# Kernel optimization log

Hardware: AMD Instinct MI355X
Metric: run time of the kernel (lower is better)

Reference implementation:

```python
import jax, jax.numpy as jnp
import numpy as np

# ---- fixed constants from stft2hcfp.__init__ ----
FS = 16000.0; FR = 2.0; FC = 27.5; TC = 1.0 / 4487.0; NPO = 48
N = int(FS / FR)                      # 8000 FFT length
HALF_N = int(round(N / 2))            # 4000
SQRT_N = float(np.sqrt(N))
HIGH_FREQ_IDX = int(round(1.0 / TC / FR) + 1)   # 2245
HIGH_QUEF_IDX = int(round(FS / FC)) + 1         # 583
CUT_Q = int(round(FS * TC))           # 4  (cepstrum cutoff)
TOTAL_BINS = 4 * 88                   # 352 log-freq bins
NUM_HARMONIC = 5

def _central_freqs():
    stop = 1.0 / TC
    nest = int(np.ceil(np.log2(stop / FC)) * NPO)
    cf = []
    for i in range(nest):
        c = FC * 2.0 ** (float(i) / NPO)
        if c < stop:
            cf.append(c)
        else:
            break
    return cf

CF = _central_freqs()   # 353 central frequencies
NEST = len(CF)

def _freq_matrix():
    # triangular log-frequency filterbank over linear freq axis
    f = (FS * np.linspace(0, 0.5, HALF_N, endpoint=True))[:HIGH_FREQ_IDX]
    W = np.zeros((NEST - 1, len(f)), np.float32)
    for i in range(1, NEST - 1):
        l = int(round(CF[i - 1] / FR)); r = int(round(CF[i + 1] / FR) + 1)
        if l >= r - 1:
            W[i, l] = 1.0
        else:
            for j in range(l, r):
                if CF[i - 1] < f[j] < CF[i]:
                    W[i, j] = (f[j] - CF[i - 1]) / (CF[i] - CF[i - 1])
                elif CF[i] < f[j] < CF[i + 1]:
                    W[i, j] = (CF[i + 1] - f[j]) / (CF[i + 1] - CF[i])
    return W

def _quef_matrix():
    q = np.arange(HIGH_QUEF_IDX) / FS + 1e-6
    fq = 1.0 / q
    W = np.zeros((NEST - 1, len(fq)), np.float32)
    for i in range(1, NEST - 1):
        for j in range(int(round(FS / CF[i + 1])), int(round(FS / CF[i - 1]) + 1)):
            if j >= len(fq):
                continue
            if CF[i - 1] < fq[j] < CF[i]:
                W[i, j] = (fq[j] - CF[i - 1]) / (CF[i] - CF[i - 1])
            elif CF[i] < fq[j] < CF[i + 1]:
                W[i, j] = (CF[i + 1] - fq[j]) / (CF[i + 1] - CF[i])
    return W

# harmonic shift indices: closest central freq to (k+1)*27.5 Hz, k=0..5
HIDS = [int(np.argmin(np.abs(np.asarray(CF) - (k + 1) * FC))) for k in range(NUM_HARMONIC + 1)]


def _nonlinear(x, g, cutoff):
    # relu + pow(g), then zero first/last `cutoff` rows along axis 1.
    # safe pow: grad is 0 where x<=0 (matches relu-masked torch behavior, no inf at 0)
    y = jnp.where(x > 0, jnp.where(x > 0, x, 1.0) ** g, 0.0)
    y = y.at[:, :cutoff].set(0.0).at[:, -cutoff:].set(0.0)
    return y


def setup_inputs() -> dict:
    key = jax.random.key(0)
    dx = jax.random.uniform(key, (8, 512, N), dtype=jnp.float32)  # [B, T, 8000] spectrogram
    return {
        "dx": dx,
        "W_freq": jnp.asarray(_freq_matrix()),   # [352, 2245]
        "W_quef": jnp.asarray(_quef_matrix()),   # [352, 583]
    }


def reference(dx, W_freq, W_quef):
    tfr0 = jnp.swapaxes(dx, 1, 2)                       # [B, F=8000, T]
    # CFP layer 1: real part of FFT over freq axis -> cepstrum, nonlinear g=0.6
    ceps = jnp.fft.fft(tfr0, axis=1).real / SQRT_N      # [B, 8000, T]
    ceps = _nonlinear(ceps, 0.6, CUT_Q)
    # log-frequency mappings (banded triangular filterbanks)
    tfr0h = tfr0[:, :HIGH_FREQ_IDX]                      # [B, 2245, T]
    cepsh = ceps[:, :HIGH_QUEF_IDX]                      # [B, 583, T]
    tfrL0 = jnp.einsum('kf,bft->bkt', W_freq, tfr0h)     # [B, 352, T]
    tfrLQ = jnp.einsum('kq,bqt->bkt', W_quef, cepsh)     # [B, 352, T]
    # harmonic stacking: shift down (spectral) / shift up (cepstral)
    har_s = [jnp.pad(tfrL0[:, h:TOTAL_BINS], ((0, 0), (0, h), (0, 0))) for h in HIDS]
    har_c = [jnp.pad(tfrLQ[:, :TOTAL_BINS - h], ((0, 0), (h, 0), (0, 0))) for h in HIDS]
    piece = jnp.concatenate([jnp.stack(har_s, axis=1), jnp.stack(har_c, axis=1)], axis=1)
    return jnp.swapaxes(piece, 2, 3)                     # [B, 12, T, 352]
```

## Files before the change

kernel.cpp:

```cpp
#include <hip/hip_runtime.h>
#include <hip/hip_bf16.h>
#include <limits.h>

typedef __attribute__((ext_vector_type(8))) short short8;
typedef __attribute__((ext_vector_type(4))) float f32x4;
typedef __attribute__((ext_vector_type(16))) float f32x16;

#define NN 8000
#define NCOL 4096
#define KBINS 352
#define QPAD 640
#define QH 320
#define BN 256
#define KC 8
#define NTILE 64
#define KSTEP 8
#define CUTQ 4
#define T_ 512
#define WFB 64
#define WQB 20
#define NGC 2560

#define GLL16(g, l) __builtin_amdgcn_global_load_lds( \
    (const __attribute__((address_space(1))) unsigned int*)(g), \
    (__attribute__((address_space(3))) unsigned int*)(l), 16, 0, 0)

static __device__ __forceinline__ ushort bfc(float f){
  __hip_bfloat16 h = __float2bfloat16(f);
  return *reinterpret_cast<ushort*>(&h);
}
static __device__ __forceinline__ float b2f(ushort u){
  unsigned v = ((unsigned)u) << 16; float f; __builtin_memcpy(&f, &v, 4); return f;
}

#define PADI(j) ((j) + ((j) >> 5))

__global__ __launch_bounds__(512) void prep_k(const float* __restrict__ dx,
        ushort* __restrict__ xf, ushort* __restrict__ cosg,
        const float* __restrict__ Wf, const float* __restrict__ Wq,
        int HFI, int HQI, int* __restrict__ fLo, int* __restrict__ qLo,
        float* __restrict__ WfT, float* __restrict__ WqT){
  __shared__ float sbuf[4232];
  __shared__ int slo, shi;
  int bid = blockIdx.x;
  int t = threadIdx.x;

  if (bid < NCOL){
    int row = bid;
    const float* rp = dx + (size_t)row*NN;
    {
      int j0 = t*8;
      f32x4 v0 = *(const f32x4*)(rp + 3896 + j0);
      f32x4 v1 = *(const f32x4*)(rp + 3896 + j0 + 4);
      #pragma unroll
      for (int e=0;e<4;e++) sbuf[PADI(j0+e)] = v0[e];
      #pragma unroll
      for (int e=0;e<4;e++) sbuf[PADI(j0+4+e)] = v1[e];
      if (t == 0){
        #pragma unroll
        for (int e=0;e<8;e++) sbuf[PADI(4096+e)] = rp[7992+e];
      }
    }
    __syncthreads();
    int n0 = t*8;
    f32x4 p0 = *(const f32x4*)(rp + n0);
    f32x4 p1 = *(const f32x4*)(rp + n0 + 4);
    float pr[8] = {p0[0],p0[1],p0[2],p0[3],p1[0],p1[1],p1[2],p1[3]};
    short8 o;
    #pragma unroll
    for (int e=0;e<8;e++){
      int n = n0 + e;
      float v;
      if (n == 0)          v = pr[0];
      else if (n < 4000)   v = pr[e] + sbuf[PADI(4104 - n)];
      else if (n == 4000)  v = pr[e];
      else                 v = 0.f;
      o[e] = (short)bfc(v);
    }
    int kt = n0 >> 6, s8 = (n0 >> 3) & 7;
    *(short8*)(&xf[((size_t)kt*NCOL + row)*64 + ((s8 ^ (row & 7)) << 3)]) = o;
  } else if (bid < NCOL + NGC){
    int base = (bid - NCOL) * 1024;
    #pragma unroll
    for (int u2=0;u2<2;u2++){
      int id = base + u2*512 + t;
      int q = id >> 12, n = id & 4095;
      float v = 0.f;
      if (q < HQI){
        int m = (q*n) % NN;
        v = cosf((float)m * 7.8539816339744831e-4f);
      }
      int kt = n >> 6, s8 = (n >> 3) & 7, e = n & 7;
      cosg[(size_t)kt*(QPAD*64) + (size_t)q*64 + (((s8 ^ (q & 7)) << 3) | e)] = bfc(v);
    }
  } else {
    int u = bid - NCOL - NGC;
    int r = u >> 1;
    bool isF = (u & 1) == 0;
    const float* W = isF ? Wf : Wq;
    int width = isF ? HFI : HQI;
    int bw    = isF ? WFB : WQB;
    float* WT = isF ? WfT : WqT;
    int* Lo   = isF ? fLo : qLo;
    if (t==0){ slo = INT_MAX; shi = -1; }
    __syncthreads();
    int mylo = INT_MAX, myhi = -1;
    for (int c = t; c < width; c += 512){
      if (W[(size_t)r*width + c] != 0.f){ if (c < mylo) mylo = c; if (c > myhi) myhi = c; }
    }
    atomicMin(&slo, mylo); atomicMax(&shi, myhi);
    __syncthreads();
    int l = (shi < 0) ? 0 : slo, h = (shi < 0) ? 0 : shi + 1;
    if (t==0) Lo[r] = l;
    for (int j = t; j < bw; j += 512){
      float v = 0.f;
      if (l + j < h) v = W[(size_t)r*width + l + j];
      WT[(size_t)j*KBINS + r] = v;
    }
  }
}

__global__ __launch_bounds__(512, 2) void gemm_k(const ushort* __restrict__ xf,
                                                 const ushort* __restrict__ cosg,
                                                 ushort* __restrict__ part){
  __shared__ ushort As[2][QH*64];
  __shared__ ushort Bs[2][BN*64];
  int tid = threadIdx.x;
  int nb = blockIdx.x, qh = blockIdx.y, kc = blockIdx.z;
  int lane = tid & 63, widx = tid >> 6;
  int wm = widx & 1, wn = widx >> 1;
  int l31 = lane & 31, lh = lane >> 5;
  int kt0 = kc*KSTEP, ktE = kt0 + KSTEP;

  const ushort* ag0 = cosg + (size_t)qh*(QH*64) + tid*8;
  const ushort* bg0 = xf + (size_t)nb*(BN*64) + tid*8;

  #define STAGE(kt_, buf_) { \
    const ushort* ag_ = ag0 + (size_t)(kt_)*(QPAD*64); \
    _Pragma("unroll") \
    for (int i_=0;i_<5;i_++) GLL16(ag_ + i_*4096, &As[buf_][tid*8 + i_*4096]); \
    const ushort* bg_ = bg0 + (size_t)(kt_)*(NCOL*64); \
    _Pragma("unroll") \
    for (int i_=0;i_<4;i_++) GLL16(bg_ + i_*4096, &Bs[buf_][tid*8 + i_*4096]); }

  f32x16 acc[5][2];
  #pragma unroll
  for (int a=0;a<5;a++){ acc[a][0] = (f32x16)0.f; acc[a][1] = (f32x16)0.f; }

  STAGE(kt0, 0);

  int cur = 0;
  for (int kt = kt0; kt < ktE; ++kt){
    if (kt + 1 < ktE){
      STAGE(kt+1, cur^1);
      asm volatile("s_waitcnt vmcnt(9)" ::: "memory");
    } else {
      asm volatile("s_waitcnt vmcnt(0)" ::: "memory");
    }
    __builtin_amdgcn_s_barrier();
    __builtin_amdgcn_sched_barrier(0);
    const ushort* Ac = &As[cur][0];
    const ushort* Bc = &Bs[cur][0];
    #pragma unroll
    for (int p=0;p<4;p++){
      short8 dfr[2];
      #pragma unroll
      for (int c=0;c<2;c++){
        int row = wn*64 + c*32 + l31;
        dfr[c] = *(const short8*)(Bc + row*64 + ((((p<<1)|lh) ^ (row & 7)) << 3));
      }
      short8 cfr[5];
      #pragma unroll
      for (int a=0;a<5;a++){
        int row = wm*160 + a*32 + l31;
        cfr[a] = *(const short8*)(Ac + row*64 + ((((p<<1)|lh) ^ (row & 7)) << 3));
      }
      __builtin_amdgcn_s_setprio(1);
      #pragma unroll
      for (int a=0;a<5;a++){
        acc[a][0] = __builtin_amdgcn_mfma_f32_32x32x16_bf16(dfr[0], cfr[a], acc[a][0], 0,0,0);
        acc[a][1] = __builtin_amdgcn_mfma_f32_32x32x16_bf16(dfr[1], cfr[a], acc[a][1], 0,0,0);
      }
      __builtin_amdgcn_s_setprio(0);
      __builtin_amdgcn_sched_barrier(0);
      __builtin_amdgcn_s_barrier();
      __builtin_amdgcn_sched_barrier(0);
    }
    cur ^= 1;
  }

  ushort* pb = part + (size_t)kc*NCOL*QPAD;
  #pragma unroll
  for (int a=0;a<5;a++){
    int q = qh*QH + wm*160 + a*32 + l31;
    #pragma unroll
    for (int c=0;c<2;c++){
      int colb = nb*BN + wn*64 + c*32 + 4*lh;
      #pragma unroll
      for (int r=0;r<16;r++){
        int col = colb + (r&3) + 8*(r>>2);
        pb[(size_t)col*QPAD + q] = bfc(acc[a][c][r]);
      }
    }
  }
}

__global__ __launch_bounds__(384) void fuse_k(const float* __restrict__ dx,
        const ushort* __restrict__ part,
        const float* __restrict__ WfT, const float* __restrict__ WqT,
        const int* __restrict__ fLo, const int* __restrict__ qLo,
        float* __restrict__ out, int HFI, int HQI){
  __shared__ float xr[2368];
  __shared__ float yq[QPAD];
  __shared__ float tl0[KBINS];
  __shared__ float tlq[KBINS];
  int col = blockIdx.x;
  int b = col >> 9, t = col & 511;
  int tid = threadIdx.x;
  const float invs = 0.011180339887498949f;

  for (int f = tid; f < 2368; f += 384) xr[f] = (f < HFI) ? dx[(size_t)col*NN + f] : 0.f;
  const ushort* pc = part + (size_t)col*QPAD;
  for (int q = tid; q < QPAD; q += 384){
    float y = 0.f;
    if (q < HQI){
      float s = 0.f;
      #pragma unroll
      for (int kc=0; kc<KC; kc++) s += b2f(pc[(size_t)kc*NCOL*QPAD + q]);
      s *= invs;
      if (q >= CUTQ && s > 0.f) y = powf(s, 0.6f);
    }
    yq[q] = y;
  }
  __syncthreads();

  if (tid < KBINS){
    int k = tid;
    int lo = fLo[k];
    float aF = 0.f;
    #pragma unroll
    for (int j=0;j<WFB;j++) aF += WfT[j*KBINS + k] * xr[lo + j];
    int ql = qLo[k];
    float aQ = 0.f;
    #pragma unroll
    for (int j=0;j<WQB;j++) aQ += WqT[j*KBINS + k] * yq[ql + j];
    tl0[k] = aF; tlq[k] = aQ;
  }
  __syncthreads();

  const int hids[6] = {0,48,76,96,111,124};
  for (int u = tid; u < 12*KBINS; u += 384){
    int j = u / KBINS;
    int k = u - j*KBINS;
    int h = hids[(j < 6) ? j : j - 6];
    float v;
    if (j < 6) v = (k + h < KBINS) ? tl0[k + h] : 0.f;
    else       v = (k >= h)        ? tlq[k - h] : 0.f;
    out[(((size_t)b*12 + j)*T_ + t)*KBINS + k] = v;
  }
}

extern "C" void kernel_launch(void* const* d_in, const int* in_sizes, int n_in,
                              void* d_out, int out_size, void* d_ws, size_t ws_size,
                              hipStream_t stream){
  const float* dx = (const float*)d_in[0];
  const float* Wf = (const float*)d_in[1];
  const float* Wq = (const float*)d_in[2];
  int HFI = in_sizes[1] / KBINS;
  int HQI = in_sizes[2] / KBINS;
  float* out = (float*)d_out;
  char* ws = (char*)d_ws;

  ushort* cosg = (ushort*)ws;
  size_t off = (size_t)NTILE*QPAD*64*2;
  ushort* xf = (ushort*)(ws + off); off += (size_t)NTILE*NCOL*64*2;
  ushort* part = (ushort*)(ws + off); off += (size_t)KC*NCOL*QPAD*2;
  int* fLo = (int*)(ws+off); off += KBINS*4;
  int* qLo = (int*)(ws+off); off += KBINS*4;
  float* WfT = (float*)(ws+off); off += (size_t)WFB*KBINS*4;
  float* WqT = (float*)(ws+off); off += (size_t)WQB*KBINS*4;
  (void)n_in; (void)out_size; (void)ws_size;

  prep_k<<<NCOL + NGC + 2*KBINS, 512, 0, stream>>>(dx, xf, cosg, Wf, Wq,
                                                   HFI, HQI, fLo, qLo, WfT, WqT);
  gemm_k<<<dim3(NCOL/BN, QPAD/QH, KC), 512, 0, stream>>>(xf, cosg, part);
  fuse_k<<<NCOL, 384, 0, stream>>>(dx, part, WfT, WqT, fLo, qLo, out, HFI, HQI);
}
```

Before: 128.5 us.

## Split prep kernel into cosine, fold, and band-prep kernels with LDS-staged fold

Breaks the monolithic prep kernel into three launches: cosine table generation, an input fold kernel, and filterbank band extraction. The fold kernel now reads the mirrored half directly from global memory with vector loads, with no per-row shared buffer. It handles 8 rows per block and stages the output in LDS, so each write to the tiled xf layout is a contiguous 1KB segment instead of scattered 16-byte stores. The aim is better write coalescing and less branch divergence between block types. The cost is two extra kernel launches.

```diff
diff --git a/kernel.cpp b/kernel.cpp
--- a/kernel.cpp
+++ b/kernel.cpp
@@ -19,7 +19,7 @@
 #define T_ 512
 #define WFB 64
 #define WQB 20
-#define NGC 2560
+#define LTS 528
 
 #define GLL16(g, l) __builtin_amdgcn_global_load_lds( \
     (const __attribute__((address_space(1))) unsigned int*)(g), \
@@ -33,90 +33,87 @@
   unsigned v = ((unsigned)u) << 16; float f; __builtin_memcpy(&f, &v, 4); return f;
 }
 
-#define PADI(j) ((j) + ((j) >> 5))
-
-__global__ __launch_bounds__(512) void prep_k(const float* __restrict__ dx,
-        ushort* __restrict__ xf, ushort* __restrict__ cosg,
-        const float* __restrict__ Wf, const float* __restrict__ Wq,
-        int HFI, int HQI, int* __restrict__ fLo, int* __restrict__ qLo,
-        float* __restrict__ WfT, float* __restrict__ WqT){
-  __shared__ float sbuf[4232];
-  __shared__ int slo, shi;
-  int bid = blockIdx.x;
+__global__ void gen_cos_k(ushort* __restrict__ cosg, int HQI){
+  int n = blockIdx.x*256 + threadIdx.x;
+  int q = blockIdx.y;
+  float v = 0.f;
+  if (q < HQI){
+    int m = (q*n) % NN;
+    v = cosf((float)m * 7.8539816339744831e-4f);
+  }
+  int kt = n >> 6, s8 = (n >> 3) & 7, e = n & 7;
+  cosg[(size_t)kt*(QPAD*64) + (size_t)q*64 + (((s8 ^ (q & 7)) << 3) | e)] = bfc(v);
+}
+
+__global__ __launch_bounds__(512, 2) void fold_k(const float* __restrict__ dx,
+                                                 ushort* __restrict__ xf){
+  __shared__ ushort lbuf[NTILE*LTS];
+  int rg = blockIdx.x;
   int t = threadIdx.x;
-
-  if (bid < NCOL){
-    int row = bid;
-    const float* rp = dx + (size_t)row*NN;
-    {
-      int j0 = t*8;
-      f32x4 v0 = *(const f32x4*)(rp + 3896 + j0);
-      f32x4 v1 = *(const f32x4*)(rp + 3896 + j0 + 4);
-      #pragma unroll
-      for (int e=0;e<4;e++) sbuf[PADI(j0+e)] = v0[e];
-      #pragma unroll
-      for (int e=0;e<4;e++) sbuf[PADI(j0+4+e)] = v1[e];
-      if (t == 0){
-        #pragma unroll
-        for (int e=0;e<8;e++) sbuf[PADI(4096+e)] = rp[7992+e];
-      }
-    }
-    __syncthreads();
-    int n0 = t*8;
+  int w = t >> 6, l = t & 63;
+  int row = rg*8 + w;
+  const float* rp = dx + (size_t)row*NN;
+  int swz = (row & 7) << 3;
+
+  #pragma unroll
+  for (int sub=0; sub<8; ++sub){
+    int n0 = sub*512 + l*8;
     f32x4 p0 = *(const f32x4*)(rp + n0);
     f32x4 p1 = *(const f32x4*)(rp + n0 + 4);
+    f32x4 ma = *(const f32x4*)(rp + 7996 - n0);
+    f32x4 mb = *(const f32x4*)(rp + 7992 - n0);
+    float ms = rp[n0 ? NN - n0 : 0];
     float pr[8] = {p0[0],p0[1],p0[2],p0[3],p1[0],p1[1],p1[2],p1[3]};
+    float mi[8] = {n0 ? ms : 0.f, ma[3],ma[2],ma[1],ma[0],mb[3],mb[2],mb[1]};
     short8 o;
     #pragma unroll
     for (int e=0;e<8;e++){
       int n = n0 + e;
       float v;
       if (n == 0)          v = pr[0];
-      else if (n < 4000)   v = pr[e] + sbuf[PADI(4104 - n)];
+      else if (n < 4000)   v = pr[e] + mi[e];
       else if (n == 4000)  v = pr[e];
       else                 v = 0.f;
       o[e] = (short)bfc(v);
     }
-    int kt = n0 >> 6, s8 = (n0 >> 3) & 7;
-    *(short8*)(&xf[((size_t)kt*NCOL + row)*64 + ((s8 ^ (row & 7)) << 3)]) = o;
-  } else if (bid < NCOL + NGC){
-    int base = (bid - NCOL) * 1024;
-    #pragma unroll
-    for (int u2=0;u2<2;u2++){
-      int id = base + u2*512 + t;
-      int q = id >> 12, n = id & 4095;
-      float v = 0.f;
-      if (q < HQI){
-        int m = (q*n) % NN;
-        v = cosf((float)m * 7.8539816339744831e-4f);
-      }
-      int kt = n >> 6, s8 = (n >> 3) & 7, e = n & 7;
-      cosg[(size_t)kt*(QPAD*64) + (size_t)q*64 + (((s8 ^ (q & 7)) << 3) | e)] = bfc(v);
-    }
-  } else {
-    int u = bid - NCOL - NGC;
-    int r = u >> 1;
-    bool isF = (u & 1) == 0;
-    const float* W = isF ? Wf : Wq;
-    int width = isF ? HFI : HQI;
-    int bw    = isF ? WFB : WQB;
-    float* WT = isF ? WfT : WqT;
-    int* Lo   = isF ? fLo : qLo;
-    if (t==0){ slo = INT_MAX; shi = -1; }
-    __syncthreads();
-    int mylo = INT_MAX, myhi = -1;
-    for (int c = t; c < width; c += 512){
-      if (W[(size_t)r*width + c] != 0.f){ if (c < mylo) mylo = c; if (c > myhi) myhi = c; }
-    }
-    atomicMin(&slo, mylo); atomicMax(&shi, myhi);
-    __syncthreads();
-    int l = (shi < 0) ? 0 : slo, h = (shi < 0) ? 0 : shi + 1;
-    if (t==0) Lo[r] = l;
-    for (int j = t; j < bw; j += 512){
-      float v = 0.f;
-      if (l + j < h) v = W[(size_t)r*width + l + j];
-      WT[(size_t)j*KBINS + r] = v;
-    }
+    int kt = n0 >> 6, s8 = n0 & 56;
+    *(short8*)(&lbuf[kt*LTS + w*64 + (s8 ^ swz)]) = o;
+  }
+  __syncthreads();
+
+  #pragma unroll
+  for (int j=0;j<8;++j){
+    int kt = j*8 + w;
+    short8 v = *(const short8*)(&lbuf[kt*LTS + l*8]);
+    *(short8*)(&xf[((size_t)kt*NCOL + rg*8)*64 + l*8]) = v;
+  }
+}
+
+__global__ void bp_k(const float* __restrict__ Wf, const float* __restrict__ Wq,
+                     int HFI, int HQI, int* __restrict__ fLo, int* __restrict__ qLo,
+                     float* __restrict__ WfT, float* __restrict__ WqT){
+  __shared__ int slo, shi;
+  int r = blockIdx.x;
+  bool isF = (blockIdx.y == 0);
+  const float* W = isF ? Wf : Wq;
+  int width = isF ? HFI : HQI;
+  int bw    = isF ? WFB : WQB;
+  float* WT = isF ? WfT : WqT;
+  int* Lo   = isF ? fLo : qLo;
+  if (threadIdx.x==0){ slo = INT_MAX; shi = -1; }
+  __syncthreads();
+  int mylo = INT_MAX, myhi = -1;
+  for (int c = threadIdx.x; c < width; c += 256){
+    if (W[(size_t)r*width + c] != 0.f){ if (c < mylo) mylo = c; if (c > myhi) myhi = c; }
+  }
+  atomicMin(&slo, mylo); atomicMax(&shi, myhi);
+  __syncthreads();
+  int l = (shi < 0) ? 0 : slo, h = (shi < 0) ? 0 : shi + 1;
+  if (threadIdx.x==0) Lo[r] = l;
+  for (int j = threadIdx.x; j < bw; j += 256){
+    float v = 0.f;
+    if (l + j < h) v = W[(size_t)r*width + l + j];
+    WT[(size_t)j*KBINS + r] = v;
   }
 }
 
@@ -281,8 +278,9 @@
   float* WqT = (float*)(ws+off); off += (size_t)WQB*KBINS*4;
   (void)n_in; (void)out_size; (void)ws_size;
 
-  prep_k<<<NCOL + NGC + 2*KBINS, 512, 0, stream>>>(dx, xf, cosg, Wf, Wq,
-                                                   HFI, HQI, fLo, qLo, WfT, WqT);
+  gen_cos_k<<<dim3(16, QPAD), 256, 0, stream>>>(cosg, HQI);
+  fold_k<<<NCOL/8, 512, 0, stream>>>(dx, xf);
+  bp_k<<<dim3(KBINS, 2), 256, 0, stream>>>(Wf, Wq, HFI, HQI, fLo, qLo, WfT, WqT);
   gemm_k<<<dim3(NCOL/BN, QPAD/QH, KC), 512, 0, stream>>>(xf, cosg, part);
   fuse_k<<<NCOL, 384, 0, stream>>>(dx, part, WfT, WqT, fLo, qLo, out, HFI, HQI);
 }
```

Result: slower. 135.5 us (+5.4%).
